# Performance work log

Hardware: AMD Instinct MI355X
Metric: run time of the kernel (lower is better)

The kernel has to match this reference:

```python
import jax, jax.numpy as jnp
import numpy as np

B, N, D, DS, LAT, FD, NF = 2, 384, 128, 3, 256, 1, 2
NPOS = DS * (2 * 5 + 1)  # 3 + 3*2*5 = 33
FREQS = np.linspace(1.0, 32.0, 5)  # torch.linspace(1, 2**5, 5)
EPS = 1e-5


def _bn(x, g, b):
    # BatchNorm1d, train-mode batch stats: normalize per channel over (batch, points)
    m = jnp.mean(x, axis=(0, 1))
    v = jnp.var(x, axis=(0, 1))
    return (x - m) * jax.lax.rsqrt(v + EPS) * g + b


def _tblock(xyz4, f, Wq, Wk, Wv, Wg1, bg1, Wg2, bg2, Wpe, bpe, g, b):
    # group_all=True full vector attention. f: [B,n,D], xyz4: [B,n,3]
    q = f @ Wq.T
    k = f @ Wk.T
    v = f @ Wv.T
    # knn_xyz gathered under no_grad in torch -> stop_gradient on the key side
    pd = xyz4[:, :, None] - jax.lax.stop_gradient(xyz4)[:, None]  # [B,n,n,3]
    parts = [pd]
    for fr in FREQS:
        parts.append(jnp.sin(pd * fr))
        parts.append(jnp.cos(pd * fr))
    pos = jnp.concatenate(parts, axis=-1) @ Wpe.T + bpe  # [B,n,n,D]
    edges = q[:, :, None] - k[:, None] + pos  # [B,n,n,D]
    h = jax.nn.relu(edges @ Wg1.T + bg1)
    attn = jax.nn.softmax(h @ Wg2.T + bg2, axis=-2)  # softmax over neighbor axis
    res = jnp.sum(attn * (v[:, None] + pos), axis=2)  # einsum bmnf,bmnf->bmf
    return _bn(res + f, g, b)


def setup_inputs() -> dict:
    key = jax.random.key(0)
    ks = iter(jax.random.split(key, 40))
    def rn(shape, s=0.05):
        return jax.random.normal(next(ks), shape, dtype=jnp.float32) * s
    z = lambda *s: jnp.zeros(s, jnp.float32)
    o = lambda *s: jnp.ones(s, jnp.float32)
    nb = NF + 1  # begin block + nfinal blocks
    return {
        "xyz": jax.random.normal(next(ks), (B, N, DS), dtype=jnp.float32),
        "feats": jax.random.normal(next(ks), (B, N, FD), dtype=jnp.float32),
        "enc_W": rn((D, FD)), "enc_b": z(D),
        "tb_Wq": rn((nb, D, D)), "tb_Wk": rn((nb, D, D)), "tb_Wv": rn((nb, D, D)),
        "tb_Wg1": rn((nb, D, D)), "tb_bg1": z(nb, D),
        "tb_Wg2": rn((nb, D, D)), "tb_bg2": z(nb, D),
        "tb_Wpe": rn((nb, D, NPOS)), "tb_bpe": z(nb, D),
        "tb_gamma": o(nb, D), "tb_beta": z(nb, D),
        "em_W1": rn((NF, D, D)), "em_b1": z(NF, D),
        "em_W2": rn((NF, D, D)), "em_b2": z(NF, D),
        "em_gamma": o(NF, D), "em_beta": z(NF, D),
        "fcf_W1": rn((LAT, D)), "fcf_b1": z(LAT),
        "fcf_W2": rn((LAT, LAT)), "fcf_b2": z(LAT),
    }


def reference(xyz, feats, enc_W, enc_b, tb_Wq, tb_Wk, tb_Wv, tb_Wg1, tb_bg1,
              tb_Wg2, tb_bg2, tb_Wpe, tb_bpe, tb_gamma, tb_beta,
              em_W1, em_b1, em_W2, em_b2, em_gamma, em_beta,
              fcf_W1, fcf_b1, fcf_W2, fcf_b2):
    f = feats @ enc_W.T + enc_b  # enc_feats
    x4 = xyz * 4.0
    for i in range(NF + 1):  # i=0: transformer_begin; i>=1: final transformers
        f = _tblock(x4, f, tb_Wq[i], tb_Wk[i], tb_Wv[i], tb_Wg1[i], tb_bg1[i],
                    tb_Wg2[i], tb_bg2[i], tb_Wpe[i], tb_bpe[i], tb_gamma[i], tb_beta[i])
        if i > 0:
            j = i - 1  # ElementwiseMLP: bn(x + relu(conv2(relu(conv1(x)))))
            y = jax.nn.relu(f @ em_W1[j].T + em_b1[j])
            y = jax.nn.relu(y @ em_W2[j].T + em_b2[j])
            f = _bn(f + y, em_gamma[j], em_beta[j])
    e = jax.nn.relu(f @ fcf_W1.T + fcf_b1) @ fcf_W2.T + fcf_b2
    return jnp.max(e, axis=1)  # lat_rep [B, lat_dim]
```

## Files before the change

kernel.cpp:

```cpp
#include <hip/hip_runtime.h>
#include <hip/hip_bf16.h>
#include <math.h>

#define B_ 2
#define N_ 384
#define D_ 128
#define LAT_ 256
#define NPOS_ 33
#define ROWS_ (B_*N_)

typedef __attribute__((ext_vector_type(8))) short bf16x8;
typedef __attribute__((ext_vector_type(4))) float f32x4;

#define MFMA(a,b,c) __builtin_amdgcn_mfma_f32_16x16x32_bf16((a),(b),(c),0,0,0)

__device__ __forceinline__ unsigned short f2bf(float x) {
    unsigned int u = __float_as_uint(x);
    u += 0x7FFFu + ((u >> 16) & 1u);
    return (unsigned short)(u >> 16);
}

__global__ __launch_bounds__(256) void enc_kernel(const float* __restrict__ feats,
                           const float* __restrict__ W,
                           const float* __restrict__ bias,
                           float* __restrict__ f) {
    int i = blockIdx.x*256 + threadIdx.x;
    if (i >= ROWS_*D_) return;
    int r = i >> 7, d = i & 127;
    f[i] = feats[r]*W[d] + bias[d];
}

__global__ __launch_bounds__(128) void qkv_kernel(const float* __restrict__ f,
    const float* __restrict__ Wq, const float* __restrict__ Wk, const float* __restrict__ Wv,
    float* __restrict__ q, float* __restrict__ k, float* __restrict__ v) {
    __shared__ float row[D_];
    int r = blockIdx.x, d = threadIdx.x;
    row[d] = f[r*D_+d];
    __syncthreads();
    float aq=0.f, ak=0.f, av=0.f;
    #pragma unroll 8
    for (int e=0;e<D_;e++){
        float x = row[e];
        aq += Wq[d*D_+e]*x;
        ak += Wk[d*D_+e]*x;
        av += Wv[d*D_+e]*x;
    }
    q[r*D_+d]=aq; k[r*D_+d]=ak; v[r*D_+d]=av;
}

__global__ __launch_bounds__(512) void attn_mfma_kernel(
    const float* __restrict__ xyz, const float* __restrict__ f,
    const float* __restrict__ qb, const float* __restrict__ kb, const float* __restrict__ vb,
    const float* __restrict__ Wpe, const float* __restrict__ bpe,
    const float* __restrict__ Wg1, const float* __restrict__ bg1,
    const float* __restrict__ Wg2, const float* __restrict__ bg2,
    float* __restrict__ gout)
{
    __shared__ unsigned short sParts[32*64];
    __shared__ unsigned short sX[32*128];
    __shared__ unsigned short sH[32*128];
    __shared__ float sK[32*132];
    __shared__ float sV[32*132];
    __shared__ float sRed[4*128];

    const int t   = threadIdx.x;
    const int w   = t >> 6;
    const int l   = t & 63;
    const int lr  = l & 15;
    const int lg  = l >> 4;
    const int rb  = w >> 2;
    const int ct0 = (w & 3) * 2;

    const int row  = blockIdx.x;
    const int b    = row / N_;
    const int brow = b * N_;

    bf16x8 bWg1[2][4], bWg2[2][4], bWpe[2][2];
    float  bpe_c[2], bg1_c[2], bg2_c[2], q_c[2];

    #pragma unroll
    for (int ct = 0; ct < 2; ++ct) {
        const int dout = (ct0 + ct) * 16 + lr;
        #pragma unroll
        for (int kt = 0; kt < 4; ++kt) {
            const float* p1 = Wg1 + dout * D_ + kt * 32 + lg * 8;
            const float* p2 = Wg2 + dout * D_ + kt * 32 + lg * 8;
            float4 a0 = *(const float4*)(p1);
            float4 a1 = *(const float4*)(p1 + 4);
            float4 c0 = *(const float4*)(p2);
            float4 c1 = *(const float4*)(p2 + 4);
            bf16x8 v1, v2;
            v1[0]=(short)f2bf(a0.x); v1[1]=(short)f2bf(a0.y); v1[2]=(short)f2bf(a0.z); v1[3]=(short)f2bf(a0.w);
            v1[4]=(short)f2bf(a1.x); v1[5]=(short)f2bf(a1.y); v1[6]=(short)f2bf(a1.z); v1[7]=(short)f2bf(a1.w);
            v2[0]=(short)f2bf(c0.x); v2[1]=(short)f2bf(c0.y); v2[2]=(short)f2bf(c0.z); v2[3]=(short)f2bf(c0.w);
            v2[4]=(short)f2bf(c1.x); v2[5]=(short)f2bf(c1.y); v2[6]=(short)f2bf(c1.z); v2[7]=(short)f2bf(c1.w);
            bWg1[ct][kt] = v1;
            bWg2[ct][kt] = v2;
        }
        #pragma unroll
        for (int kt = 0; kt < 2; ++kt) {
            bf16x8 vv;
            #pragma unroll
            for (int e = 0; e < 8; ++e) {
                const int p = kt*32 + lg*8 + e;
                const float x = (p < NPOS_) ? Wpe[dout*NPOS_ + p] : 0.f;
                vv[e] = (short)f2bf(x);
            }
            bWpe[ct][kt] = vv;
        }
        bpe_c[ct] = bpe[dout];
        bg1_c[ct] = bg1[dout];
        bg2_c[ct] = bg2[dout];
        q_c[ct]   = qb[row*D_ + dout];
    }

    const float x4m0 = 4.f*xyz[row*3+0];
    const float x4m1 = 4.f*xyz[row*3+1];
    const float x4m2 = 4.f*xyz[row*3+2];

    for (int i = t; i < 32*64/2; i += 512) ((unsigned int*)sParts)[i] = 0u;
    __syncthreads();

    float res_p[2] = {0.f, 0.f}, s_p[2] = {0.f, 0.f};

    for (int it = 0; it < N_/32; ++it) {
        const int n0 = it * 32;

        for (int s4 = t; s4 < 1024; s4 += 512) {
            const int n = s4 >> 5, c4 = s4 & 31;
            const float4 kk = *(const float4*)(kb + (brow + n0 + n)*D_ + c4*4);
            const float4 vv = *(const float4*)(vb + (brow + n0 + n)*D_ + c4*4);
            *(float4*)&sK[n*132 + c4*4] = kk;
            *(float4*)&sV[n*132 + c4*4] = vv;
        }
        {
            const int n = t >> 4, j = t & 15;
            const int nr = (brow + n0 + n) * 3;
            const float pd0 = x4m0 - 4.f*xyz[nr+0];
            const float pd1 = x4m1 - 4.f*xyz[nr+1];
            const float pd2 = x4m2 - 4.f*xyz[nr+2];
            auto pval = [&](int p) -> float {
                if (p < 3) return p==0?pd0:(p==1?pd1:pd2);
                const int qq = p - 3;
                const int fi = qq / 6;
                int rem = qq - fi*6;
                bool is_sin = true;
                if (rem >= 3) { rem -= 3; is_sin = false; }
                const float pdj = rem==0?pd0:(rem==1?pd1:pd2);
                const float fr = fi==0?1.f:(fi==1?8.75f:(fi==2?16.5f:(fi==3?24.25f:32.f)));
                const float a = pdj * fr;
                return is_sin ? __sinf(a) : __cosf(a);
            };
            const int sw = (n & 7) << 3;
            sParts[(n*64 + j)      ^ sw] = f2bf(pval(j));
            sParts[(n*64 + j + 16) ^ sw] = f2bf(pval(j + 16));
            if (j == 0) sParts[(n*64 + 32) ^ sw] = f2bf(pval(32));
        }
        __syncthreads();

        f32x4 pos[2];
        #pragma unroll
        for (int ct = 0; ct < 2; ++ct) {
            f32x4 acc = {0.f, 0.f, 0.f, 0.f};
            #pragma unroll
            for (int kt = 0; kt < 2; ++kt) {
                const int r16 = rb*16 + lr;
                const int idx = (r16*64 + kt*32 + lg*8) ^ ((r16 & 7) << 3);
                bf16x8 a = *(const bf16x8*)&sParts[idx];
                acc = MFMA(a, bWpe[ct][kt], acc);
            }
            #pragma unroll
            for (int r = 0; r < 4; ++r) acc[r] += bpe_c[ct];
            pos[ct] = acc;
        }
        #pragma unroll
        for (int ct = 0; ct < 2; ++ct) {
            const int d = (ct0 + ct)*16 + lr;
            #pragma unroll
            for (int r = 0; r < 4; ++r) {
                const int nl = rb*16 + lg*4 + r;
                const float e = pos[ct][r] + q_c[ct] - sK[nl*132 + d];
                sX[(nl*128 + d) ^ ((nl & 7) << 3)] = f2bf(e);
            }
        }
        __syncthreads();

        f32x4 hacc[2];
        hacc[0] = (f32x4){bg1_c[0], bg1_c[0], bg1_c[0], bg1_c[0]};
        hacc[1] = (f32x4){bg1_c[1], bg1_c[1], bg1_c[1], bg1_c[1]};
        #pragma unroll
        for (int kt = 0; kt < 4; ++kt) {
            const int r16 = rb*16 + lr;
            const int idx = (r16*128 + kt*32 + lg*8) ^ ((r16 & 7) << 3);
            bf16x8 a = *(const bf16x8*)&sX[idx];
            hacc[0] = MFMA(a, bWg1[0][kt], hacc[0]);
            hacc[1] = MFMA(a, bWg1[1][kt], hacc[1]);
        }
        #pragma unroll
        for (int ct = 0; ct < 2; ++ct) {
            const int d = (ct0 + ct)*16 + lr;
            #pragma unroll
            for (int r = 0; r < 4; ++r) {
                const int nl = rb*16 + lg*4 + r;
                sH[(nl*128 + d) ^ ((nl & 7) << 3)] = f2bf(fmaxf(hacc[ct][r], 0.f));
            }
        }
        __syncthreads();

        f32x4 lacc[2];
        lacc[0] = (f32x4){bg2_c[0], bg2_c[0], bg2_c[0], bg2_c[0]};
        lacc[1] = (f32x4){bg2_c[1], bg2_c[1], bg2_c[1], bg2_c[1]};
        #pragma unroll
        for (int kt = 0; kt < 4; ++kt) {
            const int r16 = rb*16 + lr;
            const int idx = (r16*128 + kt*32 + lg*8) ^ ((r16 & 7) << 3);
            bf16x8 a = *(const bf16x8*)&sH[idx];
            lacc[0] = MFMA(a, bWg2[0][kt], lacc[0]);
            lacc[1] = MFMA(a, bWg2[1][kt], lacc[1]);
        }
        #pragma unroll
        for (int ct = 0; ct < 2; ++ct) {
            const int d = (ct0 + ct)*16 + lr;
            #pragma unroll
            for (int r = 0; r < 4; ++r) {
                const int nl = rb*16 + lg*4 + r;
                const float wgt = __expf(lacc[ct][r]);
                const float vp = sV[nl*132 + d] + pos[ct][r];
                res_p[ct] += wgt * vp;
                s_p[ct]   += wgt;
            }
        }
        __syncthreads();
    }

    #pragma unroll
    for (int ct = 0; ct < 2; ++ct) {
        #pragma unroll
        for (int off = 16; off < 64; off <<= 1) {
            res_p[ct] += __shfl_xor(res_p[ct], off, 64);
            s_p[ct]   += __shfl_xor(s_p[ct], off, 64);
        }
    }
    if (lg < 2) {
        const int d = (ct0 + lg)*16 + lr;
        sRed[(rb*2+0)*128 + d] = (lg == 0) ? res_p[0] : res_p[1];
        sRed[(rb*2+1)*128 + d] = (lg == 0) ? s_p[0]   : s_p[1];
    }
    __syncthreads();
    if (t < D_) {
        const float rsum = sRed[t]       + sRed[2*128 + t];
        const float ssum = sRed[128 + t] + sRed[3*128 + t];
        gout[row*D_ + t] = rsum / ssum + f[row*D_ + t];
    }
}

__global__ __launch_bounds__(256) void bn_kernel(const float* __restrict__ g,
    const float* __restrict__ gamma, const float* __restrict__ beta,
    float* __restrict__ fout)
{
    __shared__ float ssum[256], ssq[256];
    int d = blockIdx.x, t = threadIdx.x;
    float s=0.f, sq=0.f;
    for (int r=t; r<ROWS_; r+=256){ float x = g[r*D_+d]; s+=x; sq+=x*x; }
    ssum[t]=s; ssq[t]=sq; __syncthreads();
    for (int off=128; off>0; off>>=1){
        if (t<off){ ssum[t]+=ssum[t+off]; ssq[t]+=ssq[t+off]; }
        __syncthreads();
    }
    float mean = ssum[0]*(1.f/ROWS_);
    float var  = ssq[0]*(1.f/ROWS_) - mean*mean;
    float rs   = rsqrtf(var + 1e-5f);
    float ga = gamma[d], be = beta[d];
    for (int r=t; r<ROWS_; r+=256){
        fout[r*D_+d] = (g[r*D_+d]-mean)*rs*ga + be;
    }
}

__global__ __launch_bounds__(128) void em_kernel(const float* __restrict__ f,
    const float* __restrict__ W1, const float* __restrict__ b1,
    const float* __restrict__ W2, const float* __restrict__ b2,
    float* __restrict__ gout)
{
    __shared__ float row[D_], y1[D_];
    int r = blockIdx.x, d = threadIdx.x;
    row[d] = f[r*D_+d]; __syncthreads();
    float a = b1[d];
    #pragma unroll 8
    for (int e=0;e<D_;e++) a += W1[d*D_+e]*row[e];
    y1[d] = fmaxf(a,0.f); __syncthreads();
    float a2 = b2[d];
    #pragma unroll 8
    for (int e=0;e<D_;e++) a2 += W2[d*D_+e]*y1[e];
    a2 = fmaxf(a2,0.f);
    gout[r*D_+d] = row[d] + a2;
}

__global__ __launch_bounds__(256) void final_kernel(const float* __restrict__ f,
    const float* __restrict__ W1, const float* __restrict__ b1,
    const float* __restrict__ W2, const float* __restrict__ b2,
    float* __restrict__ e_ws)
{
    __shared__ float row[D_];
    __shared__ float h1[LAT_];
    int r = blockIdx.x, t = threadIdx.x;
    if (t < D_) row[t] = f[r*D_+t];
    __syncthreads();
    float a = b1[t];
    #pragma unroll 8
    for (int e=0;e<D_;e++) a += W1[t*D_+e]*row[e];
    h1[t] = fmaxf(a,0.f);
    __syncthreads();
    float a2 = b2[t];
    #pragma unroll 8
    for (int e=0;e<LAT_;e++) a2 += W2[t*LAT_+e]*h1[e];
    e_ws[r*LAT_+t] = a2;
}

__global__ __launch_bounds__(256) void maxred_kernel(const float* __restrict__ e_ws,
                                                     float* __restrict__ out)
{
    int b = blockIdx.x, l = threadIdx.x;
    float m = -INFINITY;
    for (int n=0;n<N_;n++) m = fmaxf(m, e_ws[(b*N_+n)*LAT_+l]);
    out[b*LAT_+l] = m;
}

extern "C" void kernel_launch(void* const* d_in, const int* in_sizes, int n_in,
                              void* d_out, int out_size, void* d_ws, size_t ws_size,
                              hipStream_t stream) {
    (void)in_sizes; (void)n_in; (void)out_size; (void)ws_size;
    const float* xyz    = (const float*)d_in[0];
    const float* feats  = (const float*)d_in[1];
    const float* enc_W  = (const float*)d_in[2];
    const float* enc_b  = (const float*)d_in[3];
    const float* tb_Wq  = (const float*)d_in[4];
    const float* tb_Wk  = (const float*)d_in[5];
    const float* tb_Wv  = (const float*)d_in[6];
    const float* tb_Wg1 = (const float*)d_in[7];
    const float* tb_bg1 = (const float*)d_in[8];
    const float* tb_Wg2 = (const float*)d_in[9];
    const float* tb_bg2 = (const float*)d_in[10];
    const float* tb_Wpe = (const float*)d_in[11];
    const float* tb_bpe = (const float*)d_in[12];
    const float* tb_gamma = (const float*)d_in[13];
    const float* tb_beta  = (const float*)d_in[14];
    const float* em_W1  = (const float*)d_in[15];
    const float* em_b1  = (const float*)d_in[16];
    const float* em_W2  = (const float*)d_in[17];
    const float* em_b2  = (const float*)d_in[18];
    const float* em_gamma = (const float*)d_in[19];
    const float* em_beta  = (const float*)d_in[20];
    const float* fcf_W1 = (const float*)d_in[21];
    const float* fcf_b1 = (const float*)d_in[22];
    const float* fcf_W2 = (const float*)d_in[23];
    const float* fcf_b2 = (const float*)d_in[24];
    float* out = (float*)d_out;

    float* ws = (float*)d_ws;
    float* fbuf = ws;
    float* gbuf = fbuf + ROWS_*D_;
    float* qbuf = gbuf + ROWS_*D_;
    float* kbuf = qbuf + ROWS_*D_;
    float* vbuf = kbuf + ROWS_*D_;
    float* ebuf = vbuf + ROWS_*D_;

    enc_kernel<<<(ROWS_*D_+255)/256, 256, 0, stream>>>(feats, enc_W, enc_b, fbuf);

    for (int i = 0; i < 3; i++) {
        const float* Wq  = tb_Wq  + i*D_*D_;
        const float* Wk  = tb_Wk  + i*D_*D_;
        const float* Wv  = tb_Wv  + i*D_*D_;
        const float* Wg1 = tb_Wg1 + i*D_*D_;
        const float* bg1 = tb_bg1 + i*D_;
        const float* Wg2 = tb_Wg2 + i*D_*D_;
        const float* bg2 = tb_bg2 + i*D_;
        const float* Wpe = tb_Wpe + i*D_*NPOS_;
        const float* bpe = tb_bpe + i*D_;

        qkv_kernel<<<ROWS_, 128, 0, stream>>>(fbuf, Wq, Wk, Wv, qbuf, kbuf, vbuf);
        attn_mfma_kernel<<<ROWS_, 512, 0, stream>>>(xyz, fbuf, qbuf, kbuf, vbuf,
                                                    Wpe, bpe, Wg1, bg1, Wg2, bg2, gbuf);
        bn_kernel<<<D_, 256, 0, stream>>>(gbuf, tb_gamma + i*D_, tb_beta + i*D_, fbuf);

        if (i > 0) {
            int j = i - 1;
            em_kernel<<<ROWS_, 128, 0, stream>>>(fbuf, em_W1 + j*D_*D_, em_b1 + j*D_,
                                                 em_W2 + j*D_*D_, em_b2 + j*D_, gbuf);
            bn_kernel<<<D_, 256, 0, stream>>>(gbuf, em_gamma + j*D_, em_beta + j*D_, fbuf);
        }
    }

    final_kernel<<<ROWS_, 256, 0, stream>>>(fbuf, fcf_W1, fcf_b1, fcf_W2, fcf_b2, ebuf);
    maxred_kernel<<<B_, 256, 0, stream>>>(ebuf, out);
}
```

Before: 617.0 us.

## Fuse batchnorm into neighbouring kernels via atomic stats and restructure attention loop

Removes the standalone batchnorm kernels. Producers now accumulate per-channel sum and sum-of-squares with atomics, and consumers apply the normalization on load. The attention kernel drops its shared-memory K/V staging in favour of direct global reads, and software-pipelines position/edge generation for the next tile after the current tile's work. The matvec kernels switch to float4 weight loads. This trades fewer launches and less LDS traffic for atomic contention on 256 addresses per kernel, uncoalesced global K/V reads, and a one-pass variance formula that is less numerically stable.

```diff
diff --git a/kernel.cpp b/kernel.cpp
--- a/kernel.cpp
+++ b/kernel.cpp
@@ -1,6 +1,5 @@
 #include <hip/hip_runtime.h>
 #include <hip/hip_bf16.h>
-#include <math.h>
 
 #define B_ 2
 #define N_ 384
@@ -18,6 +17,14 @@
     unsigned int u = __float_as_uint(x);
     u += 0x7FFFu + ((u >> 16) & 1u);
     return (unsigned short)(u >> 16);
+}
+
+__device__ __forceinline__ float bn_apply(float x, const float* stats, const float* gam,
+                                          const float* bet, int d) {
+    float s  = stats[d], sq = stats[128 + d];
+    float mean = s * (1.f/ROWS_);
+    float var  = sq * (1.f/ROWS_) - mean*mean;
+    return (x - mean) * rsqrtf(var + 1e-5f) * gam[d] + bet[d];
 }
 
 __global__ __launch_bounds__(256) void enc_kernel(const float* __restrict__ feats,
@@ -30,37 +37,44 @@
     f[i] = feats[r]*W[d] + bias[d];
 }
 
-__global__ __launch_bounds__(128) void qkv_kernel(const float* __restrict__ f,
+__global__ __launch_bounds__(128) void qkv_kernel(const float* __restrict__ graw,
+    const float* __restrict__ stats, const float* __restrict__ gam, const float* __restrict__ bet,
+    int use_stats,
     const float* __restrict__ Wq, const float* __restrict__ Wk, const float* __restrict__ Wv,
     float* __restrict__ q, float* __restrict__ k, float* __restrict__ v) {
     __shared__ float row[D_];
     int r = blockIdx.x, d = threadIdx.x;
-    row[d] = f[r*D_+d];
+    float x = graw[r*D_+d];
+    if (use_stats) x = bn_apply(x, stats, gam, bet, d);
+    row[d] = x;
     __syncthreads();
     float aq=0.f, ak=0.f, av=0.f;
-    #pragma unroll 8
-    for (int e=0;e<D_;e++){
-        float x = row[e];
-        aq += Wq[d*D_+e]*x;
-        ak += Wk[d*D_+e]*x;
-        av += Wv[d*D_+e]*x;
+    #pragma unroll 4
+    for (int e4=0;e4<D_/4;e4++){
+        float4 wq = *(const float4*)(Wq + d*D_ + e4*4);
+        float4 wk = *(const float4*)(Wk + d*D_ + e4*4);
+        float4 wv = *(const float4*)(Wv + d*D_ + e4*4);
+        float x0=row[e4*4+0], x1=row[e4*4+1], x2=row[e4*4+2], x3=row[e4*4+3];
+        aq += wq.x*x0 + wq.y*x1 + wq.z*x2 + wq.w*x3;
+        ak += wk.x*x0 + wk.y*x1 + wk.z*x2 + wk.w*x3;
+        av += wv.x*x0 + wv.y*x1 + wv.z*x2 + wv.w*x3;
     }
     q[r*D_+d]=aq; k[r*D_+d]=ak; v[r*D_+d]=av;
 }
 
 __global__ __launch_bounds__(512) void attn_mfma_kernel(
-    const float* __restrict__ xyz, const float* __restrict__ f,
+    const float* __restrict__ xyz, const float* __restrict__ graw,
+    const float* __restrict__ stats_in, const float* __restrict__ gam_in,
+    const float* __restrict__ bet_in, int use_stats,
     const float* __restrict__ qb, const float* __restrict__ kb, const float* __restrict__ vb,
     const float* __restrict__ Wpe, const float* __restrict__ bpe,
     const float* __restrict__ Wg1, const float* __restrict__ bg1,
     const float* __restrict__ Wg2, const float* __restrict__ bg2,
-    float* __restrict__ gout)
+    float* __restrict__ gout, float* __restrict__ stats_out)
 {
     __shared__ unsigned short sParts[32*64];
     __shared__ unsigned short sX[32*128];
     __shared__ unsigned short sH[32*128];
-    __shared__ float sK[32*132];
-    __shared__ float sV[32*132];
     __shared__ float sRed[4*128];
 
     const int t   = threadIdx.x;
@@ -121,44 +135,32 @@
     for (int i = t; i < 32*64/2; i += 512) ((unsigned int*)sParts)[i] = 0u;
     __syncthreads();
 
-    float res_p[2] = {0.f, 0.f}, s_p[2] = {0.f, 0.f};
-
-    for (int it = 0; it < N_/32; ++it) {
-        const int n0 = it * 32;
-
-        for (int s4 = t; s4 < 1024; s4 += 512) {
-            const int n = s4 >> 5, c4 = s4 & 31;
-            const float4 kk = *(const float4*)(kb + (brow + n0 + n)*D_ + c4*4);
-            const float4 vv = *(const float4*)(vb + (brow + n0 + n)*D_ + c4*4);
-            *(float4*)&sK[n*132 + c4*4] = kk;
-            *(float4*)&sV[n*132 + c4*4] = vv;
-        }
-        {
-            const int n = t >> 4, j = t & 15;
-            const int nr = (brow + n0 + n) * 3;
-            const float pd0 = x4m0 - 4.f*xyz[nr+0];
-            const float pd1 = x4m1 - 4.f*xyz[nr+1];
-            const float pd2 = x4m2 - 4.f*xyz[nr+2];
-            auto pval = [&](int p) -> float {
-                if (p < 3) return p==0?pd0:(p==1?pd1:pd2);
-                const int qq = p - 3;
-                const int fi = qq / 6;
-                int rem = qq - fi*6;
-                bool is_sin = true;
-                if (rem >= 3) { rem -= 3; is_sin = false; }
-                const float pdj = rem==0?pd0:(rem==1?pd1:pd2);
-                const float fr = fi==0?1.f:(fi==1?8.75f:(fi==2?16.5f:(fi==3?24.25f:32.f)));
-                const float a = pdj * fr;
-                return is_sin ? __sinf(a) : __cosf(a);
-            };
-            const int sw = (n & 7) << 3;
-            sParts[(n*64 + j)      ^ sw] = f2bf(pval(j));
-            sParts[(n*64 + j + 16) ^ sw] = f2bf(pval(j + 16));
-            if (j == 0) sParts[(n*64 + 32) ^ sw] = f2bf(pval(32));
-        }
-        __syncthreads();
-
-        f32x4 pos[2];
+    auto partsgen = [&](int n0) {
+        const int n = t >> 4, j = t & 15;
+        const int nr = (brow + n0 + n) * 3;
+        const float pd0 = x4m0 - 4.f*xyz[nr+0];
+        const float pd1 = x4m1 - 4.f*xyz[nr+1];
+        const float pd2 = x4m2 - 4.f*xyz[nr+2];
+        auto pval = [&](int p) -> float {
+            if (p < 3) return p==0?pd0:(p==1?pd1:pd2);
+            const int qq = p - 3;
+            const int fi = qq / 6;
+            int rem = qq - fi*6;
+            bool is_sin = true;
+            if (rem >= 3) { rem -= 3; is_sin = false; }
+            const float pdj = rem==0?pd0:(rem==1?pd1:pd2);
+            const float fr = fi==0?1.f:(fi==1?8.75f:(fi==2?16.5f:(fi==3?24.25f:32.f)));
+            const float a = pdj * fr;
+            return is_sin ? __sinf(a) : __cosf(a);
+        };
+        const int sw = (n & 7) << 3;
+        sParts[(n*64 + j)      ^ sw] = f2bf(pval(j));
+        sParts[(n*64 + j + 16) ^ sw] = f2bf(pval(j + 16));
+        if (j == 0) sParts[(n*64 + 32) ^ sw] = f2bf(pval(32));
+    };
+
+    f32x4 pos[2];
+    auto posedges = [&](int n0) {
         #pragma unroll
         for (int ct = 0; ct < 2; ++ct) {
             f32x4 acc = {0.f, 0.f, 0.f, 0.f};
@@ -179,11 +181,21 @@
             #pragma unroll
             for (int r = 0; r < 4; ++r) {
                 const int nl = rb*16 + lg*4 + r;
-                const float e = pos[ct][r] + q_c[ct] - sK[nl*132 + d];
+                const float e = pos[ct][r] + q_c[ct] - kb[(brow + n0 + nl)*D_ + d];
                 sX[(nl*128 + d) ^ ((nl & 7) << 3)] = f2bf(e);
             }
         }
-        __syncthreads();
+    };
+
+    partsgen(0);
+    __syncthreads();
+    posedges(0);
+    __syncthreads();
+
+    float res_p[2] = {0.f, 0.f}, s_p[2] = {0.f, 0.f};
+
+    for (int it = 0; it < N_/32; ++it) {
+        const int n0 = it * 32;
 
         f32x4 hacc[2];
         hacc[0] = (f32x4){bg1_c[0], bg1_c[0], bg1_c[0], bg1_c[0]};
@@ -225,12 +237,18 @@
             for (int r = 0; r < 4; ++r) {
                 const int nl = rb*16 + lg*4 + r;
                 const float wgt = __expf(lacc[ct][r]);
-                const float vp = sV[nl*132 + d] + pos[ct][r];
+                const float vp = vb[(brow + n0 + nl)*D_ + d] + pos[ct][r];
                 res_p[ct] += wgt * vp;
                 s_p[ct]   += wgt;
             }
         }
+        if (it < N_/32 - 1) partsgen(n0 + 32);
         __syncthreads();
+
+        if (it < N_/32 - 1) {
+            posedges(n0 + 32);
+            __syncthreads();
+        }
     }
 
     #pragma unroll
@@ -250,52 +268,47 @@
     if (t < D_) {
         const float rsum = sRed[t]       + sRed[2*128 + t];
         const float ssum = sRed[128 + t] + sRed[3*128 + t];
-        gout[row*D_ + t] = rsum / ssum + f[row*D_ + t];
-    }
-}
-
-__global__ __launch_bounds__(256) void bn_kernel(const float* __restrict__ g,
-    const float* __restrict__ gamma, const float* __restrict__ beta,
-    float* __restrict__ fout)
-{
-    __shared__ float ssum[256], ssq[256];
-    int d = blockIdx.x, t = threadIdx.x;
-    float s=0.f, sq=0.f;
-    for (int r=t; r<ROWS_; r+=256){ float x = g[r*D_+d]; s+=x; sq+=x*x; }
-    ssum[t]=s; ssq[t]=sq; __syncthreads();
-    for (int off=128; off>0; off>>=1){
-        if (t<off){ ssum[t]+=ssum[t+off]; ssq[t]+=ssq[t+off]; }
-        __syncthreads();
-    }
-    float mean = ssum[0]*(1.f/ROWS_);
-    float var  = ssq[0]*(1.f/ROWS_) - mean*mean;
-    float rs   = rsqrtf(var + 1e-5f);
-    float ga = gamma[d], be = beta[d];
-    for (int r=t; r<ROWS_; r+=256){
-        fout[r*D_+d] = (g[r*D_+d]-mean)*rs*ga + be;
-    }
-}
-
-__global__ __launch_bounds__(128) void em_kernel(const float* __restrict__ f,
+        float fres = graw[row*D_ + t];
+        if (use_stats) fres = bn_apply(fres, stats_in, gam_in, bet_in, t);
+        const float val = rsum / ssum + fres;
+        gout[row*D_ + t] = val;
+        atomicAdd(&stats_out[t], val);
+        atomicAdd(&stats_out[128 + t], val*val);
+    }
+}
+
+__global__ __launch_bounds__(128) void em_kernel(const float* __restrict__ graw,
+    const float* __restrict__ stats_in, const float* __restrict__ gam_in, const float* __restrict__ bet_in,
     const float* __restrict__ W1, const float* __restrict__ b1,
     const float* __restrict__ W2, const float* __restrict__ b2,
-    float* __restrict__ gout)
+    float* __restrict__ gout, float* __restrict__ stats_out)
 {
     __shared__ float row[D_], y1[D_];
     int r = blockIdx.x, d = threadIdx.x;
-    row[d] = f[r*D_+d]; __syncthreads();
+    float fn = bn_apply(graw[r*D_+d], stats_in, gam_in, bet_in, d);
+    row[d] = fn; __syncthreads();
     float a = b1[d];
-    #pragma unroll 8
-    for (int e=0;e<D_;e++) a += W1[d*D_+e]*row[e];
+    #pragma unroll 4
+    for (int e4=0;e4<D_/4;e4++){
+        float4 w = *(const float4*)(W1 + d*D_ + e4*4);
+        a += w.x*row[e4*4+0] + w.y*row[e4*4+1] + w.z*row[e4*4+2] + w.w*row[e4*4+3];
+    }
     y1[d] = fmaxf(a,0.f); __syncthreads();
     float a2 = b2[d];
-    #pragma unroll 8
-    for (int e=0;e<D_;e++) a2 += W2[d*D_+e]*y1[e];
+    #pragma unroll 4
+    for (int e4=0;e4<D_/4;e4++){
+        float4 w = *(const float4*)(W2 + d*D_ + e4*4);
+        a2 += w.x*y1[e4*4+0] + w.y*y1[e4*4+1] + w.z*y1[e4*4+2] + w.w*y1[e4*4+3];
+    }
     a2 = fmaxf(a2,0.f);
-    gout[r*D_+d] = row[d] + a2;
-}
-
-__global__ __launch_bounds__(256) void final_kernel(const float* __restrict__ f,
+    const float g2 = fn + a2;
+    gout[r*D_+d] = g2;
+    atomicAdd(&stats_out[d], g2);
+    atomicAdd(&stats_out[128+d], g2*g2);
+}
+
+__global__ __launch_bounds__(256) void final_kernel(const float* __restrict__ graw,
+    const float* __restrict__ stats_in, const float* __restrict__ gam_in, const float* __restrict__ bet_in,
     const float* __restrict__ W1, const float* __restrict__ b1,
     const float* __restrict__ W2, const float* __restrict__ b2,
     float* __restrict__ e_ws)
@@ -303,16 +316,22 @@
     __shared__ float row[D_];
     __shared__ float h1[LAT_];
     int r = blockIdx.x, t = threadIdx.x;
-    if (t < D_) row[t] = f[r*D_+t];
+    if (t < D_) row[t] = bn_apply(graw[r*D_+t], stats_in, gam_in, bet_in, t);
     __syncthreads();
     float a = b1[t];
-    #pragma unroll 8
-    for (int e=0;e<D_;e++) a += W1[t*D_+e]*row[e];
+    #pragma unroll 4
+    for (int e4=0;e4<D_/4;e4++){
+        float4 w = *(const float4*)(W1 + t*D_ + e4*4);
+        a += w.x*row[e4*4+0] + w.y*row[e4*4+1] + w.z*row[e4*4+2] + w.w*row[e4*4+3];
+    }
     h1[t] = fmaxf(a,0.f);
     __syncthreads();
     float a2 = b2[t];
-    #pragma unroll 8
-    for (int e=0;e<LAT_;e++) a2 += W2[t*LAT_+e]*h1[e];
+    #pragma unroll 4
+    for (int e4=0;e4<LAT_/4;e4++){
+        float4 w = *(const float4*)(W2 + t*LAT_ + e4*4);
+        a2 += w.x*h1[e4*4+0] + w.y*h1[e4*4+1] + w.z*h1[e4*4+2] + w.w*h1[e4*4+3];
+    }
     e_ws[r*LAT_+t] = a2;
 }
 
@@ -321,6 +340,7 @@
 {
     int b = blockIdx.x, l = threadIdx.x;
     float m = -INFINITY;
+    #pragma unroll 8
     for (int n=0;n<N_;n++) m = fmaxf(m, e_ws[(b*N_+n)*LAT_+l]);
     out[b*LAT_+l] = m;
 }
@@ -356,40 +376,50 @@
     const float* fcf_b2 = (const float*)d_in[24];
     float* out = (float*)d_out;
 
-    float* ws = (float*)d_ws;
-    float* fbuf = ws;
-    float* gbuf = fbuf + ROWS_*D_;
-    float* qbuf = gbuf + ROWS_*D_;
+    float* ws   = (float*)d_ws;
+    float* buf0 = ws;
+    float* buf1 = buf0 + ROWS_*D_;
+    float* qbuf = buf1 + ROWS_*D_;
     float* kbuf = qbuf + ROWS_*D_;
     float* vbuf = kbuf + ROWS_*D_;
     float* ebuf = vbuf + ROWS_*D_;
-
-    enc_kernel<<<(ROWS_*D_+255)/256, 256, 0, stream>>>(feats, enc_W, enc_b, fbuf);
-
-    for (int i = 0; i < 3; i++) {
-        const float* Wq  = tb_Wq  + i*D_*D_;
-        const float* Wk  = tb_Wk  + i*D_*D_;
-        const float* Wv  = tb_Wv  + i*D_*D_;
-        const float* Wg1 = tb_Wg1 + i*D_*D_;
-        const float* bg1 = tb_bg1 + i*D_;
-        const float* Wg2 = tb_Wg2 + i*D_*D_;
-        const float* bg2 = tb_bg2 + i*D_;
-        const float* Wpe = tb_Wpe + i*D_*NPOS_;
-        const float* bpe = tb_bpe + i*D_;
-
-        qkv_kernel<<<ROWS_, 128, 0, stream>>>(fbuf, Wq, Wk, Wv, qbuf, kbuf, vbuf);
-        attn_mfma_kernel<<<ROWS_, 512, 0, stream>>>(xyz, fbuf, qbuf, kbuf, vbuf,
-                                                    Wpe, bpe, Wg1, bg1, Wg2, bg2, gbuf);
-        bn_kernel<<<D_, 256, 0, stream>>>(gbuf, tb_gamma + i*D_, tb_beta + i*D_, fbuf);
-
-        if (i > 0) {
-            int j = i - 1;
-            em_kernel<<<ROWS_, 128, 0, stream>>>(fbuf, em_W1 + j*D_*D_, em_b1 + j*D_,
-                                                 em_W2 + j*D_*D_, em_b2 + j*D_, gbuf);
-            bn_kernel<<<D_, 256, 0, stream>>>(gbuf, em_gamma + j*D_, em_beta + j*D_, fbuf);
-        }
-    }
-
-    final_kernel<<<ROWS_, 256, 0, stream>>>(fbuf, fcf_W1, fcf_b1, fcf_W2, fcf_b2, ebuf);
+    float* stats = ebuf + ROWS_*LAT_;
+    float* sA0 = stats;
+    float* sA1 = stats + 256;
+    float* sE1 = stats + 512;
+    float* sA2 = stats + 768;
+    float* sE2 = stats + 1024;
+
+    hipMemsetAsync(stats, 0, 5*256*sizeof(float), stream);
+
+    enc_kernel<<<(ROWS_*D_+255)/256, 256, 0, stream>>>(feats, enc_W, enc_b, buf0);
+
+    const float* gz = tb_gamma;
+    qkv_kernel<<<ROWS_, 128, 0, stream>>>(buf0, gz, gz, gz, 0,
+                                          tb_Wq, tb_Wk, tb_Wv, qbuf, kbuf, vbuf);
+    attn_mfma_kernel<<<ROWS_, 512, 0, stream>>>(xyz, buf0, gz, gz, gz, 0,
+        qbuf, kbuf, vbuf,
+        tb_Wpe, tb_bpe, tb_Wg1, tb_bg1, tb_Wg2, tb_bg2, buf1, sA0);
+    qkv_kernel<<<ROWS_, 128, 0, stream>>>(buf1, sA0, tb_gamma, tb_beta, 1,
+                                          tb_Wq + 1*D_*D_, tb_Wk + 1*D_*D_, tb_Wv + 1*D_*D_,
+                                          qbuf, kbuf, vbuf);
+    attn_mfma_kernel<<<ROWS_, 512, 0, stream>>>(xyz, buf1, sA0, tb_gamma, tb_beta, 1,
+        qbuf, kbuf, vbuf,
+        tb_Wpe + 1*D_*NPOS_, tb_bpe + 1*D_, tb_Wg1 + 1*D_*D_, tb_bg1 + 1*D_,
+        tb_Wg2 + 1*D_*D_, tb_bg2 + 1*D_, buf0, sA1);
+    em_kernel<<<ROWS_, 128, 0, stream>>>(buf0, sA1, tb_gamma + 1*D_, tb_beta + 1*D_,
+                                         em_W1, em_b1, em_W2, em_b2, buf1, sE1);
+    qkv_kernel<<<ROWS_, 128, 0, stream>>>(buf1, sE1, em_gamma, em_beta, 1,
+                                          tb_Wq + 2*D_*D_, tb_Wk + 2*D_*D_, tb_Wv + 2*D_*D_,
+                                          qbuf, kbuf, vbuf);
+    attn_mfma_kernel<<<ROWS_, 512, 0, stream>>>(xyz, buf1, sE1, em_gamma, em_beta, 1,
+        qbuf, kbuf, vbuf,
+        tb_Wpe + 2*D_*NPOS_, tb_bpe + 2*D_, tb_Wg1 + 2*D_*D_, tb_bg1 + 2*D_,
+        tb_Wg2 + 2*D_*D_, tb_bg2 + 2*D_, buf0, sA2);
+    em_kernel<<<ROWS_, 128, 0, stream>>>(buf0, sA2, tb_gamma + 2*D_, tb_beta + 2*D_,
+                                         em_W1 + 1*D_*D_, em_b1 + 1*D_,
+                                         em_W2 + 1*D_*D_, em_b2 + 1*D_, buf1, sE2);
+    final_kernel<<<ROWS_, 256, 0, stream>>>(buf1, sE2, em_gamma + 1*D_, em_beta + 1*D_,
+                                            fcf_W1, fcf_b1, fcf_W2, fcf_b2, ebuf);
     maxred_kernel<<<B_, 256, 0, stream>>>(ebuf, out);
 }
```

Measured after the change: 660.6 us. 1.07x slower.
